# Optimization experiments

Hardware: AMD Instinct MI355X
Metric: run time of the kernel (lower is better)

## Reference

```python
import jax, jax.numpy as jnp
import numpy as np

VOCAB = 50000
EMB = 128
B, T = 512, 128
U1, U2, U3 = 64, 32, 32


def gru_dir(x, W, U, bi, br, reverse):
    """Keras GRU, reset_after=True, recurrent_activation=sigmoid, activation=relu.
    x: [B,T,D]; W: [D,3u]; U: [u,3u]; bi, br: [3u] (gate order z, r, h)."""
    u = U.shape[0]
    if reverse:
        x = x[:, ::-1]
    xz = jnp.einsum('btd,dk->btk', x, W) + bi          # [B,T,3u] input projection
    xz_t = jnp.swapaxes(xz, 0, 1)                      # [T,B,3u]
    h0 = jnp.zeros((x.shape[0], u), x.dtype)

    def step(h, xt):
        rec = h @ U + br                               # [B,3u]
        z = jax.nn.sigmoid(xt[:, :u] + rec[:, :u])
        r = jax.nn.sigmoid(xt[:, u:2 * u] + rec[:, u:2 * u])
        hh = jax.nn.relu(xt[:, 2 * u:] + r * rec[:, 2 * u:])
        h = z * h + (1.0 - z) * hh
        return h, h

    _, hs = jax.lax.scan(step, h0, xz_t)               # [T,B,u]
    hs = jnp.swapaxes(hs, 0, 1)                        # [B,T,u]
    if reverse:
        hs = hs[:, ::-1]
    return hs


def setup_inputs() -> dict:
    key = jax.random.key(0)
    ks = iter(jax.random.split(key, 32))
    s = 0.08

    def p(shape):
        return jax.random.normal(next(ks), shape, dtype=jnp.float32) * s

    inp = {
        'x': jax.random.randint(next(ks), (B, T), 0, VOCAB, dtype=jnp.int32),
        'emb': p((VOCAB, EMB)),
        # layer 1 (input EMB=128, units 64), fwd / bwd
        'W1f': p((EMB, 3 * U1)), 'U1f': p((U1, 3 * U1)), 'bi1f': p((3 * U1,)), 'br1f': p((3 * U1,)),
        'W1b': p((EMB, 3 * U1)), 'U1b': p((U1, 3 * U1)), 'bi1b': p((3 * U1,)), 'br1b': p((3 * U1,)),
        # layer 2 (input 2*U1=128, units 32)
        'W2f': p((2 * U1, 3 * U2)), 'U2f': p((U2, 3 * U2)), 'bi2f': p((3 * U2,)), 'br2f': p((3 * U2,)),
        'W2b': p((2 * U1, 3 * U2)), 'U2b': p((U2, 3 * U2)), 'bi2b': p((3 * U2,)), 'br2b': p((3 * U2,)),
        # layer 3 (input 2*U2=64, units 32), return last state
        'W3f': p((2 * U2, 3 * U3)), 'U3f': p((U3, 3 * U3)), 'bi3f': p((3 * U3,)), 'br3f': p((3 * U3,)),
        'W3b': p((2 * U2, 3 * U3)), 'U3b': p((U3, 3 * U3)), 'bi3b': p((3 * U3,)), 'br3b': p((3 * U3,)),
        # dense softmax head (in 2*U3=64 -> VOCAB)
        'Wd': p((2 * U3, VOCAB)), 'bd': p((VOCAB,)),
    }
    return inp


def reference(x, emb, W1f, U1f, bi1f, br1f, W1b, U1b, bi1b, br1b,
              W2f, U2f, bi2f, br2f, W2b, U2b, bi2b, br2b,
              W3f, U3f, bi3f, br3f, W3b, U3b, bi3b, br3b, Wd, bd):
    h = emb[x]                                                       # [B,T,EMB]
    # bidirectional GRU 1 (return_sequences=True, concat)
    h = jnp.concatenate([gru_dir(h, W1f, U1f, bi1f, br1f, False),
                         gru_dir(h, W1b, U1b, bi1b, br1b, True)], axis=-1)
    # bidirectional GRU 2 (return_sequences=True, concat)
    h = jnp.concatenate([gru_dir(h, W2f, U2f, bi2f, br2f, False),
                         gru_dir(h, W2b, U2b, bi2b, br2b, True)], axis=-1)
    # bidirectional GRU 3 (return_sequences=False -> concat final states)
    hf = gru_dir(h, W3f, U3f, bi3f, br3f, False)[:, -1]              # fwd final
    hb = gru_dir(h, W3b, U3b, bi3b, br3b, True)[:, 0]                # bwd final (t=0 after unreversing)
    h = jnp.concatenate([hf, hb], axis=-1)                           # [B, 2*U3]
    # dropout layers are identity at inference
    return jax.nn.softmax(h @ Wd + bd, axis=-1)                      # [B, VOCAB]
```

## Files before the change

kernel.cpp:

```cpp
#include <hip/hip_runtime.h>
#include <math.h>

#define B_ 512
#define T_ 128
#define VOCAB_ 50000

template<int K, int U3, bool GATHER>
__global__ void proj_kernel(const float* __restrict__ in,
                            const int* __restrict__ idx,
                            const float* __restrict__ emb,
                            const float* __restrict__ Wf, const float* __restrict__ Wb,
                            const float* __restrict__ bif, const float* __restrict__ bib,
                            float* __restrict__ out)
{
    constexpr int TPB  = 2 * U3 / 3;
    constexpr int ROWS = 8;
    constexpr int NC   = 2 * U3;
    __shared__ float et[K * ROWS];
    const int tid = threadIdx.x;
    const long row0 = (long)blockIdx.x * ROWS;

    constexpr int F4 = K / 4;
    for (int i = tid; i < ROWS * F4; i += TPB) {
        int r = i / F4, q = i % F4;
        const float* src;
        if (GATHER) src = emb + (long)idx[row0 + r] * K + q * 4;
        else        src = in  + (row0 + r) * (long)K + q * 4;
        float4 v = *(const float4*)src;
        et[(q * 4 + 0) * ROWS + r] = v.x;
        et[(q * 4 + 1) * ROWS + r] = v.y;
        et[(q * 4 + 2) * ROWS + r] = v.z;
        et[(q * 4 + 3) * ROWS + r] = v.w;
    }
    __syncthreads();

    const float* wp[3];
    float acc[3][ROWS];
    #pragma unroll
    for (int g = 0; g < 3; g++) {
        int col = tid + g * TPB;
        const float* W  = (col < U3) ? Wf  : Wb;
        const float* bi = (col < U3) ? bif : bib;
        int cc = (col < U3) ? col : col - U3;
        wp[g] = W + cc;
        float b = bi[cc];
        #pragma unroll
        for (int r = 0; r < ROWS; r++) acc[g][r] = b;
    }

    for (int k = 0; k < K; k++) {
        float w0 = wp[0][(long)k * U3];
        float w1 = wp[1][(long)k * U3];
        float w2 = wp[2][(long)k * U3];
        const float4* e4 = (const float4*)&et[k * ROWS];
        float4 ea = e4[0], eb = e4[1];
        float ev[8] = {ea.x, ea.y, ea.z, ea.w, eb.x, eb.y, eb.z, eb.w};
        #pragma unroll
        for (int r = 0; r < ROWS; r++) {
            acc[0][r] = fmaf(ev[r], w0, acc[0][r]);
            acc[1][r] = fmaf(ev[r], w1, acc[1][r]);
            acc[2][r] = fmaf(ev[r], w2, acc[2][r]);
        }
    }

    #pragma unroll
    for (int g = 0; g < 3; g++) {
        int col = tid + g * TPB;
        for (int r = 0; r < ROWS; r++)
            out[(row0 + r) * NC + col] = acc[g][r];
    }
}

template<int U, bool WRITE_ALL>
__global__ __launch_bounds__(64, 1)
void gru_rec_kernel(const float* __restrict__ xz,
                    const float* __restrict__ Uwf, const float* __restrict__ Uwb,
                    const float* __restrict__ brf, const float* __restrict__ brb,
                    float* __restrict__ out, int NB)
{
    constexpr int U3 = 3 * U;
    constexpr int NC = 6 * U;
    const int lane = threadIdx.x;
    const int dir = blockIdx.x / NB;
    const int blk = blockIdx.x % NB;
    const float* Uw = dir ? Uwb : Uwf;
    const float* br = dir ? brb : brf;

    int kp, half;
    long batch;
    if constexpr (U == 64) { kp = lane; half = 0; batch = blk; }
    else { kp = lane & 31; half = lane >> 5; batch = (long)blk * 2 + half; }

    float wz[U], wr[U], wh[U];
    #pragma unroll
    for (int j = 0; j < U; j++) {
        wz[j] = Uw[j * U3 + kp];
        wr[j] = Uw[j * U3 + U + kp];
        wh[j] = Uw[j * U3 + 2 * U + kp];
    }
    const float brz = br[kp], brr = br[U + kp], brh = br[2 * U + kp];

    __shared__ float hsh[64];
    float h = 0.f;
    const float* xzb = xz + batch * (long)T_ * NC + dir * U3;

    auto rowp = [&](int tt) -> const float* {
        int t = dir ? (T_ - 1 - tt) : tt;
        return xzb + (long)t * NC;
    };

    const float* r0 = rowp(0);
    const float* r1 = rowp(1);
    float p0z = r0[kp], p0r = r0[U + kp], p0h = r0[2 * U + kp];
    float p1z = r1[kp], p1r = r1[U + kp], p1h = r1[2 * U + kp];

    auto step = [&](int tt, float& pz, float& pr, float& ph) {
        float xzz = pz, xzr = pr, xzh = ph;
        if (tt + 2 < T_) {
            const float* q = rowp(tt + 2);
            pz = q[kp]; pr = q[U + kp]; ph = q[2 * U + kp];
        }
        float accz = brz, accr = brr, acch = brh;

        if constexpr (U == 64) {
            #pragma unroll
            for (int j = 0; j < 64; j++) {
                float hj = __builtin_bit_cast(float,
                    __builtin_amdgcn_readlane(__builtin_bit_cast(int, h), j));
                accz = fmaf(hj, wz[j], accz);
                accr = fmaf(hj, wr[j], accr);
                acch = fmaf(hj, wh[j], acch);
            }
        } else {
            hsh[lane] = h;
            float ha[32];
            const float4* hv = (const float4*)&hsh[half * 32];
            #pragma unroll
            for (int q4 = 0; q4 < 8; q4++) {
                float4 v = hv[q4];
                ha[q4 * 4 + 0] = v.x; ha[q4 * 4 + 1] = v.y;
                ha[q4 * 4 + 2] = v.z; ha[q4 * 4 + 3] = v.w;
            }
            #pragma unroll
            for (int j = 0; j < 32; j++) {
                accz = fmaf(ha[j], wz[j], accz);
                accr = fmaf(ha[j], wr[j], accr);
                acch = fmaf(ha[j], wh[j], acch);
            }
        }

        float z = 1.f / (1.f + expf(-(xzz + accz)));
        float r = 1.f / (1.f + expf(-(xzr + accr)));
        float hh = fmaxf(xzh + r * acch, 0.f);
        h = fmaf(z, h - hh, hh);

        if (WRITE_ALL) {
            int t = dir ? (T_ - 1 - tt) : tt;
            long row = batch * T_ + t;
            out[row * (2 * U) + dir * U + kp] = h;
        }
    };

    for (int tt = 0; tt < T_; tt += 2) {
        step(tt,     p0z, p0r, p0h);
        step(tt + 1, p1z, p1r, p1h);
    }
    if (!WRITE_ALL)
        out[batch * (2 * U) + dir * U + kp] = h;
}

__global__ void dense_exp_kernel(const float* __restrict__ h3, const float* __restrict__ Wd,
                                 const float* __restrict__ bd, float* __restrict__ out,
                                 float* __restrict__ partials)
{
    constexpr int RW = 64;
    __shared__ float ht[64 * RW];
    __shared__ float red[4 * RW];
    const int tid = threadIdx.x;
    const int row0 = blockIdx.y * RW;
    const int col = blockIdx.x * 256 + tid;

    for (int i = tid; i < RW * 16; i += 256) {
        int r = i / 16, q = i % 16;
        float4 v = *(const float4*)(h3 + (long)(row0 + r) * 64 + q * 4);
        ht[(q * 4 + 0) * RW + r] = v.x;
        ht[(q * 4 + 1) * RW + r] = v.y;
        ht[(q * 4 + 2) * RW + r] = v.z;
        ht[(q * 4 + 3) * RW + r] = v.w;
    }
    __syncthreads();

    float acc[RW];
    #pragma unroll
    for (int r = 0; r < RW; r++) acc[r] = 0.f;
    const bool valid = col < VOCAB_;
    const float* wcol = Wd + col;

    for (int k = 0; k < 64; k++) {
        float w = valid ? wcol[(long)k * VOCAB_] : 0.f;
        const float4* h4 = (const float4*)&ht[k * RW];
        #pragma unroll
        for (int r4 = 0; r4 < RW / 4; r4++) {
            float4 hv = h4[r4];
            acc[r4 * 4 + 0] = fmaf(w, hv.x, acc[r4 * 4 + 0]);
            acc[r4 * 4 + 1] = fmaf(w, hv.y, acc[r4 * 4 + 1]);
            acc[r4 * 4 + 2] = fmaf(w, hv.z, acc[r4 * 4 + 2]);
            acc[r4 * 4 + 3] = fmaf(w, hv.w, acc[r4 * 4 + 3]);
        }
    }
    const float bdv = valid ? bd[col] : 0.f;
    const int lane = tid & 63, wv = tid >> 6;

    #pragma unroll
    for (int r = 0; r < RW; r++) {
        float e = valid ? expf(acc[r] + bdv) : 0.f;
        if (valid) out[(long)(row0 + r) * VOCAB_ + col] = e;
        for (int off = 32; off; off >>= 1) e += __shfl_down(e, off);
        if (lane == 0) red[wv * RW + r] = e;
    }
    __syncthreads();
    for (int r = tid; r < RW; r += 256) {
        float s = red[0 * RW + r] + red[1 * RW + r] + red[2 * RW + r] + red[3 * RW + r];
        partials[(long)blockIdx.x * B_ + row0 + r] = s;
    }
}

__global__ void rowsum_kernel(const float* __restrict__ partials,
                              float* __restrict__ rinv, int ncolblk)
{
    int row = blockIdx.x * blockDim.x + threadIdx.x;
    if (row >= B_) return;
    float s = 0.f;
    for (int p = 0; p < ncolblk; p++) s += partials[(long)p * B_ + row];
    rinv[row] = 1.f / s;
}

__global__ void scale_kernel(float* __restrict__ out, const float* __restrict__ rinv)
{
    const unsigned n4 = (unsigned)B_ * VOCAB_ / 4u;
    const unsigned c4 = VOCAB_ / 4u;
    for (unsigned i = blockIdx.x * blockDim.x + threadIdx.x; i < n4;
         i += gridDim.x * blockDim.x) {
        unsigned row = i / c4;
        float s = rinv[row];
        float4 v = ((float4*)out)[i];
        v.x *= s; v.y *= s; v.z *= s; v.w *= s;
        ((float4*)out)[i] = v;
    }
}

extern "C" void kernel_launch(void* const* d_in, const int* in_sizes, int n_in,
                              void* d_out, int out_size, void* d_ws, size_t ws_size,
                              hipStream_t stream)
{
    const int*   x    = (const int*)  d_in[0];
    const float* emb  = (const float*)d_in[1];
    const float* W1f  = (const float*)d_in[2];
    const float* U1f  = (const float*)d_in[3];
    const float* bi1f = (const float*)d_in[4];
    const float* br1f = (const float*)d_in[5];
    const float* W1b  = (const float*)d_in[6];
    const float* U1b  = (const float*)d_in[7];
    const float* bi1b = (const float*)d_in[8];
    const float* br1b = (const float*)d_in[9];
    const float* W2f  = (const float*)d_in[10];
    const float* U2f  = (const float*)d_in[11];
    const float* bi2f = (const float*)d_in[12];
    const float* br2f = (const float*)d_in[13];
    const float* W2b  = (const float*)d_in[14];
    const float* U2b  = (const float*)d_in[15];
    const float* bi2b = (const float*)d_in[16];
    const float* br2b = (const float*)d_in[17];
    const float* W3f  = (const float*)d_in[18];
    const float* U3f  = (const float*)d_in[19];
    const float* bi3f = (const float*)d_in[20];
    const float* br3f = (const float*)d_in[21];
    const float* W3b  = (const float*)d_in[22];
    const float* U3b  = (const float*)d_in[23];
    const float* bi3b = (const float*)d_in[24];
    const float* br3b = (const float*)d_in[25];
    const float* Wd   = (const float*)d_in[26];
    const float* bd   = (const float*)d_in[27];

    const long NROWS = (long)B_ * T_;
    const int  NCB   = (VOCAB_ + 255) / 256;

    float* xz = (float*)d_out;

    char* w = (char*)d_ws;
    float* h1 = (float*)w;            w += NROWS * 128 * sizeof(float);
    float* h2 = (float*)w;            w += NROWS * 64  * sizeof(float);
    float* h3 = (float*)w;            w += (long)B_ * 64 * sizeof(float);
    float* partials = (float*)w;      w += (long)NCB * B_ * sizeof(float);
    float* rinv = (float*)w;          w += B_ * sizeof(float);

    proj_kernel<128, 192, true><<<NROWS / 8, 128, 0, stream>>>(
        nullptr, x, emb, W1f, W1b, bi1f, bi1b, xz);
    gru_rec_kernel<64, true><<<1024, 64, 0, stream>>>(
        xz, U1f, U1b, br1f, br1b, h1, 512);

    proj_kernel<128, 96, false><<<NROWS / 8, 64, 0, stream>>>(
        h1, nullptr, nullptr, W2f, W2b, bi2f, bi2b, xz);
    gru_rec_kernel<32, true><<<512, 64, 0, stream>>>(
        xz, U2f, U2b, br2f, br2b, h2, 256);

    proj_kernel<64, 96, false><<<NROWS / 8, 64, 0, stream>>>(
        h2, nullptr, nullptr, W3f, W3b, bi3f, bi3b, xz);
    gru_rec_kernel<32, false><<<512, 64, 0, stream>>>(
        xz, U3f, U3b, br3f, br3b, h3, 256);

    dense_exp_kernel<<<dim3(NCB, B_ / 64), 256, 0, stream>>>(
        h3, Wd, bd, (float*)d_out, partials);
    rowsum_kernel<<<(B_ + 255) / 256, 256, 0, stream>>>(partials, rinv, NCB);
    scale_kernel<<<2048, 256, 0, stream>>>((float*)d_out, rinv);
}
```

Before: 839.0 us.

## Split GRU recurrent matvec across two waves with shared-memory partial sums

Each recurrent block now runs two wavefronts, and each wave handles half of the hidden-state reduction dimension. Partial gate sums are exchanged through LDS with a __syncthreads every timestep. A small pre-kernel transposes the recurrent weights so each lane can load its slice with float4 reads, and the accumulators are split into even and odd chains for more ILP. The aim is to halve the serial FMA chain per step, at the cost of a block barrier each step and doubled threads per block.

```diff
diff --git a/kernel.cpp b/kernel.cpp
--- a/kernel.cpp
+++ b/kernel.cpp
@@ -4,6 +4,26 @@
 #define B_ 512
 #define T_ 128
 #define VOCAB_ 50000
+
+template<int I> struct IC { static constexpr int v = I; };
+template<int I, int N, typename F>
+__device__ __forceinline__ void sfor(F f) {
+    if constexpr (I < N) { f(IC<I>{}); sfor<I + 1, N>(f); }
+}
+
+__global__ void wtrans_kernel(const float* __restrict__ Uf, const float* __restrict__ Ub,
+                              float* __restrict__ dst, int u)
+{
+    int n = 3 * u * u;
+    for (int i = blockIdx.x * blockDim.x + threadIdx.x; i < 2 * n;
+         i += gridDim.x * blockDim.x) {
+        int d = i / n, r = i % n;
+        int g = r / (u * u), rem = r % (u * u);
+        int kp = rem / u, j = rem % u;
+        const float* U = d ? Ub : Uf;
+        dst[i] = U[j * 3 * u + g * u + kp];
+    }
+}
 
 template<int K, int U3, bool GATHER>
 __global__ void proj_kernel(const float* __restrict__ in,
@@ -72,38 +92,53 @@
 }
 
 template<int U, bool WRITE_ALL>
-__global__ __launch_bounds__(64, 1)
+__global__ __launch_bounds__(128, 1)
 void gru_rec_kernel(const float* __restrict__ xz,
-                    const float* __restrict__ Uwf, const float* __restrict__ Uwb,
+                    const float* __restrict__ Ut,
                     const float* __restrict__ brf, const float* __restrict__ brb,
                     float* __restrict__ out, int NB)
 {
     constexpr int U3 = 3 * U;
     constexpr int NC = 6 * U;
-    const int lane = threadIdx.x;
-    const int dir = blockIdx.x / NB;
-    const int blk = blockIdx.x % NB;
-    const float* Uw = dir ? Uwb : Uwf;
-    const float* br = dir ? brb : brf;
+    constexpr int JW = (U == 64) ? 32 : 16;
+    constexpr int SPB = (U == 64) ? 1 : 2;
+
+    const int tid  = threadIdx.x;
+    const int w    = tid >> 6;
+    const int lane = tid & 63;
+    const int dir  = blockIdx.x / NB;
+    const int blk  = blockIdx.x % NB;
+    const float* Utd = Ut + (long)dir * 3 * U * U;
+    const float* br  = dir ? brb : brf;
 
     int kp, half;
-    long batch;
-    if constexpr (U == 64) { kp = lane; half = 0; batch = blk; }
-    else { kp = lane & 31; half = lane >> 5; batch = (long)blk * 2 + half; }
-
-    float wz[U], wr[U], wh[U];
-    #pragma unroll
-    for (int j = 0; j < U; j++) {
-        wz[j] = Uw[j * U3 + kp];
-        wr[j] = Uw[j * U3 + U + kp];
-        wh[j] = Uw[j * U3 + 2 * U + kp];
-    }
+    if constexpr (U == 64) { kp = lane; half = 0; }
+    else { kp = lane & 31; half = lane >> 5; }
+    const long batch = (long)blk * SPB + half;
+    const int j0 = w * JW;
+
+    float wz[JW], wr[JW], wh[JW];
+    sfor<0, JW / 4>([&](auto icq) {
+        constexpr int q = decltype(icq)::v;
+        float4 vz = *(const float4*)&Utd[(0 * U + kp) * U + j0 + 4 * q];
+        float4 vr = *(const float4*)&Utd[(1 * U + kp) * U + j0 + 4 * q];
+        float4 vh = *(const float4*)&Utd[(2 * U + kp) * U + j0 + 4 * q];
+        wz[4*q+0]=vz.x; wz[4*q+1]=vz.y; wz[4*q+2]=vz.z; wz[4*q+3]=vz.w;
+        wr[4*q+0]=vr.x; wr[4*q+1]=vr.y; wr[4*q+2]=vr.z; wr[4*q+3]=vr.w;
+        wh[4*q+0]=vh.x; wh[4*q+1]=vh.y; wh[4*q+2]=vh.z; wh[4*q+3]=vh.w;
+        asm volatile("" : "+v"(wz[4*q+0]), "+v"(wz[4*q+1]), "+v"(wz[4*q+2]), "+v"(wz[4*q+3]));
+        asm volatile("" : "+v"(wr[4*q+0]), "+v"(wr[4*q+1]), "+v"(wr[4*q+2]), "+v"(wr[4*q+3]));
+        asm volatile("" : "+v"(wh[4*q+0]), "+v"(wh[4*q+1]), "+v"(wh[4*q+2]), "+v"(wh[4*q+3]));
+    });
     const float brz = br[kp], brr = br[U + kp], brh = br[2 * U + kp];
 
-    __shared__ float hsh[64];
+    __shared__ float ps[2][2][3][64];
+    __shared__ float hsh[2][64];
+
     float h = 0.f;
+    if constexpr (U == 32) hsh[w][lane] = 0.f;
+
     const float* xzb = xz + batch * (long)T_ * NC + dir * U3;
-
     auto rowp = [&](int tt) -> const float* {
         int t = dir ? (T_ - 1 - tt) : tt;
         return xzb + (long)t * NC;
@@ -114,47 +149,60 @@
     float p0z = r0[kp], p0r = r0[U + kp], p0h = r0[2 * U + kp];
     float p1z = r1[kp], p1r = r1[U + kp], p1h = r1[2 * U + kp];
 
-    auto step = [&](int tt, float& pz, float& pr, float& ph) {
+    auto step = [&](int tt, int slot, float& pz, float& pr, float& ph) {
         float xzz = pz, xzr = pr, xzh = ph;
         if (tt + 2 < T_) {
             const float* q = rowp(tt + 2);
             pz = q[kp]; pr = q[U + kp]; ph = q[2 * U + kp];
         }
-        float accz = brz, accr = brr, acch = brh;
-
-        if constexpr (U == 64) {
-            #pragma unroll
-            for (int j = 0; j < 64; j++) {
-                float hj = __builtin_bit_cast(float,
-                    __builtin_amdgcn_readlane(__builtin_bit_cast(int, h), j));
-                accz = fmaf(hj, wz[j], accz);
-                accr = fmaf(hj, wr[j], accr);
-                acch = fmaf(hj, wh[j], acch);
+
+        float ha[JW];
+        if constexpr (U == 32) {
+            const float4* hv = (const float4*)&hsh[w][half * 32 + j0];
+            sfor<0, JW / 4>([&](auto icq) {
+                constexpr int q4 = decltype(icq)::v;
+                float4 v = hv[q4];
+                ha[q4*4+0]=v.x; ha[q4*4+1]=v.y; ha[q4*4+2]=v.z; ha[q4*4+3]=v.w;
+            });
+        }
+
+        float az0 = 0.f, az1 = 0.f, ar0 = 0.f, ar1 = 0.f, ah0 = 0.f, ah1 = 0.f;
+        sfor<0, JW>([&](auto ic) {
+            constexpr int jj = decltype(ic)::v;
+            float hj;
+            if constexpr (U == 64)
+                hj = __builtin_bit_cast(float,
+                    __builtin_amdgcn_readlane(__builtin_bit_cast(int, h), j0 + jj));
+            else
+                hj = ha[jj];
+            if constexpr ((jj & 1) == 0) {
+                az0 = fmaf(hj, wz[jj], az0);
+                ar0 = fmaf(hj, wr[jj], ar0);
+                ah0 = fmaf(hj, wh[jj], ah0);
+            } else {
+                az1 = fmaf(hj, wz[jj], az1);
+                ar1 = fmaf(hj, wr[jj], ar1);
+                ah1 = fmaf(hj, wh[jj], ah1);
             }
-        } else {
-            hsh[lane] = h;
-            float ha[32];
-            const float4* hv = (const float4*)&hsh[half * 32];
-            #pragma unroll
-            for (int q4 = 0; q4 < 8; q4++) {
-                float4 v = hv[q4];
-                ha[q4 * 4 + 0] = v.x; ha[q4 * 4 + 1] = v.y;
-                ha[q4 * 4 + 2] = v.z; ha[q4 * 4 + 3] = v.w;
-            }
-            #pragma unroll
-            for (int j = 0; j < 32; j++) {
-                accz = fmaf(ha[j], wz[j], accz);
-                accr = fmaf(ha[j], wr[j], accr);
-                acch = fmaf(ha[j], wh[j], acch);
-            }
-        }
+        });
+        float az = az0 + az1, ar = ar0 + ar1, ah = ah0 + ah1;
+
+        ps[slot][w][0][lane] = az;
+        ps[slot][w][1][lane] = ar;
+        ps[slot][w][2][lane] = ah;
+        __syncthreads();
+        float accz = brz + az + ps[slot][w ^ 1][0][lane];
+        float accr = brr + ar + ps[slot][w ^ 1][1][lane];
+        float acch = brh + ah + ps[slot][w ^ 1][2][lane];
 
         float z = 1.f / (1.f + expf(-(xzz + accz)));
         float r = 1.f / (1.f + expf(-(xzr + accr)));
         float hh = fmaxf(xzh + r * acch, 0.f);
         h = fmaf(z, h - hh, hh);
 
-        if (WRITE_ALL) {
+        if constexpr (U == 32) hsh[w][lane] = h;
+
+        if (WRITE_ALL && w == 0) {
             int t = dir ? (T_ - 1 - tt) : tt;
             long row = batch * T_ + t;
             out[row * (2 * U) + dir * U + kp] = h;
@@ -162,10 +210,10 @@
     };
 
     for (int tt = 0; tt < T_; tt += 2) {
-        step(tt,     p0z, p0r, p0h);
-        step(tt + 1, p1z, p1r, p1h);
-    }
-    if (!WRITE_ALL)
+        step(tt,     0, p0z, p0r, p0h);
+        step(tt + 1, 1, p1z, p1r, p1h);
+    }
+    if (!WRITE_ALL && w == 0)
         out[batch * (2 * U) + dir * U + kp] = h;
 }
 
@@ -293,21 +341,28 @@
     float* h3 = (float*)w;            w += (long)B_ * 64 * sizeof(float);
     float* partials = (float*)w;      w += (long)NCB * B_ * sizeof(float);
     float* rinv = (float*)w;          w += B_ * sizeof(float);
+    float* wsU1 = (float*)w;          w += 2L * 3 * 64 * 64 * sizeof(float);
+    float* wsU2 = (float*)w;          w += 2L * 3 * 32 * 32 * sizeof(float);
+    float* wsU3 = (float*)w;          w += 2L * 3 * 32 * 32 * sizeof(float);
+
+    wtrans_kernel<<<96, 256, 0, stream>>>(U1f, U1b, wsU1, 64);
+    wtrans_kernel<<<24, 256, 0, stream>>>(U2f, U2b, wsU2, 32);
+    wtrans_kernel<<<24, 256, 0, stream>>>(U3f, U3b, wsU3, 32);
 
     proj_kernel<128, 192, true><<<NROWS / 8, 128, 0, stream>>>(
         nullptr, x, emb, W1f, W1b, bi1f, bi1b, xz);
-    gru_rec_kernel<64, true><<<1024, 64, 0, stream>>>(
-        xz, U1f, U1b, br1f, br1b, h1, 512);
+    gru_rec_kernel<64, true><<<1024, 128, 0, stream>>>(
+        xz, wsU1, br1f, br1b, h1, 512);
 
     proj_kernel<128, 96, false><<<NROWS / 8, 64, 0, stream>>>(
         h1, nullptr, nullptr, W2f, W2b, bi2f, bi2b, xz);
-    gru_rec_kernel<32, true><<<512, 64, 0, stream>>>(
-        xz, U2f, U2b, br2f, br2b, h2, 256);
+    gru_rec_kernel<32, true><<<512, 128, 0, stream>>>(
+        xz, wsU2, br2f, br2b, h2, 256);
 
     proj_kernel<64, 96, false><<<NROWS / 8, 64, 0, stream>>>(
         h2, nullptr, nullptr, W3f, W3b, bi3f, bi3b, xz);
-    gru_rec_kernel<32, false><<<512, 64, 0, stream>>>(
-        xz, U3f, U3b, br3f, br3b, h3, 256);
+    gru_rec_kernel<32, false><<<512, 128, 0, stream>>>(
+        xz, wsU3, br3f, br3b, h3, 256);
 
     dense_exp_kernel<<<dim3(NCB, B_ / 64), 256, 0, stream>>>(
         h3, Wd, bd, (float*)d_out, partials);
```

New measurement: 881.2 us. +5.0%, slower.
